# Optimization experiments

Measured on AMD Instinct MI355X. Metric: run time of the kernel, lower is better.

## Reference

```python
import jax, jax.numpy as jnp
import numpy as np
import math

B, T, C = 2, 2048, 1024
H = 16            # n_head
RATIO = 4         # ratio_kv
HKV = H // RATIO  # n_head_kv = 4
HD = C // H       # head_dim = 64
G = H // HKV      # query heads per kv head = 4


def _alibi_slopes(n_heads):
    # n_heads must be a power of 2 here (H=16)
    assert math.log2(n_heads).is_integer()
    start = 2.0 ** (-(2.0 ** (-(math.log2(n_heads) - 3))))
    return np.array([start * (start ** i) for i in range(n_heads)], dtype=np.float32)


def setup_inputs() -> dict:
    key = jax.random.key(0)
    ks = jax.random.split(key, 5)
    return {
        "x": jax.random.normal(ks[0], (B, T, C), dtype=jnp.float32),
        "Wq": jax.random.normal(ks[1], (C, C), dtype=jnp.float32) * 0.02,
        "Wk": jax.random.normal(ks[2], (C, HKV * HD), dtype=jnp.float32) * 0.02,
        "Wv": jax.random.normal(ks[3], (C, HKV * HD), dtype=jnp.float32) * 0.02,
        "Wo": jax.random.normal(ks[4], (C, C), dtype=jnp.float32) * 0.02,
    }


def reference(x, Wq, Wk, Wv, Wo):
    # GQA causal attention with ALiBi bias (flash-disabled fallback path).
    # q: [B,HKV,G,T,HD] (grouped query heads), k/v: [B,HKV,T,HD]
    q = (x @ Wq).reshape(B, T, H, HD).transpose(0, 2, 1, 3).reshape(B, HKV, G, T, HD)
    k = (x @ Wk).reshape(B, T, HKV, HD).transpose(0, 2, 1, 3)
    v = (x @ Wv).reshape(B, T, HKV, HD).transpose(0, 2, 1, 3)

    scale = 1.0 / math.sqrt(HD)
    att = jnp.einsum('bkgtd,bksd->bkgts', q, k) * scale  # [B,HKV,G,T,T]

    # ALiBi: original repeats alibi(n_head) by G and truncates to n_head,
    # so query head h uses slope get_slopes(H)[h // G] == slopes[:HKV] per kv group.
    slopes = jnp.asarray(_alibi_slopes(H))[:HKV]          # [HKV]
    pos = jnp.arange(T)
    rel = (pos[None, :] - pos[:, None]).astype(jnp.float32)  # [T,T], rel[i,j]=j-i
    bias = slopes[:, None, None] * rel                    # [HKV,T,T]
    causal = jnp.triu(jnp.full((T, T), -jnp.inf, dtype=jnp.float32), 1)

    att = att + bias[None, :, None] + causal
    att = jax.nn.softmax(att.astype(jnp.float32), axis=-1).astype(q.dtype)

    y = jnp.einsum('bkgts,bksd->bkgtd', att, v)           # [B,HKV,G,T,HD]
    y = y.reshape(B, H, T, HD).transpose(0, 2, 1, 3).reshape(B, T, C)
    return y @ Wo
```

## Files before the change

### kernel.cpp

```cpp
#include <hip/hip_runtime.h>
#include <hip/hip_bf16.h>
#include <math.h>

#define B_ 2
#define T_ 2048
#define C_ 1024
#define H_ 16
#define HKV_ 4
#define G_ 4
#define HD_ 64
#define KVC_ 256
#define NQKV_ 1536
#define NQT_ 32

typedef __attribute__((ext_vector_type(8))) short bf16x8;
typedef __attribute__((ext_vector_type(4))) float f32x4;

static __device__ inline short f2bf(float f) {
    __hip_bfloat16 h = __float2bfloat16(f);
    short s;
    __builtin_memcpy(&s, &h, 2);
    return s;
}
static __device__ inline short f2bf_trunc(float f) {
    unsigned int u;
    __builtin_memcpy(&u, &f, 4);
    return (short)(u >> 16);
}
static __device__ inline float bf2f(short s) {
    unsigned int u = ((unsigned int)(unsigned short)s) << 16;
    float f;
    __builtin_memcpy(&f, &u, 4);
    return f;
}

static __device__ inline void gload_lds16(const short* g, short* lds) {
    __builtin_amdgcn_global_load_lds(
        (const __attribute__((address_space(1))) unsigned int*)g,
        (__attribute__((address_space(3))) unsigned int*)lds, 16, 0, 0);
}

__global__ __launch_bounds__(256) void cast_bf16(
    const float* __restrict__ in, short* __restrict__ out, int n)
{
    const int i = (blockIdx.x * 256 + threadIdx.x) * 8;
    if (i >= n) return;
    const float4 a = *(const float4*)(in + i);
    const float4 b = *(const float4*)(in + i + 4);
    bf16x8 o;
    o[0] = f2bf(a.x); o[1] = f2bf(a.y); o[2] = f2bf(a.z); o[3] = f2bf(a.w);
    o[4] = f2bf(b.x); o[5] = f2bf(b.y); o[6] = f2bf(b.z); o[7] = f2bf(b.w);
    *(bf16x8*)(out + i) = o;
}

__global__ __launch_bounds__(256) void w_transpose(
    const float* __restrict__ Wq, const float* __restrict__ Wk,
    const float* __restrict__ Wv, const float* __restrict__ Wo,
    short* __restrict__ Wt, short* __restrict__ Wot)
{
    const int z = blockIdx.z;
    const float* in;
    short* out;
    int N;
    if (z == 0)      { in = Wq; out = Wt;                     N = C_; }
    else if (z == 1) { in = Wk; out = Wt + C_ * C_;           N = KVC_; }
    else if (z == 2) { in = Wv; out = Wt + (C_ + KVC_) * C_;  N = KVC_; }
    else             { in = Wo; out = Wot;                    N = C_; }
    const int n0 = blockIdx.x * 32;
    if (n0 >= N) return;
    __shared__ float t[32][33];
    const int tx = threadIdx.x, ty = threadIdx.y;
    const int k0 = blockIdx.y * 32;
    #pragma unroll
    for (int j = 0; j < 4; j++)
        t[ty + j * 8][tx] = in[(size_t)(k0 + ty + j * 8) * N + n0 + tx];
    __syncthreads();
    #pragma unroll
    for (int j = 0; j < 4; j++)
        out[(size_t)(n0 + ty + j * 8) * C_ + k0 + tx] = f2bf(t[tx][ty + j * 8]);
}

template <bool OUT_BF16>
__global__ __launch_bounds__(256) void gemm_bf16(
    const short* __restrict__ A, const short* __restrict__ Bt,
    void* __restrict__ Cout, int M, int N, int K)
{
    __shared__ short As[2][128 * 32];
    __shared__ short Bs[2][128 * 32];
    const int tid = threadIdx.x;
    const int wave = tid >> 6, lane = tid & 63;
    const int l15 = lane & 15, quad = lane >> 4;
    const int row0 = blockIdx.y * 128, col0 = blockIdx.x * 128;
    const int wr = (wave >> 1) * 64, wc = (wave & 1) * 64;
    const int sr = lane >> 2, kof = (lane & 3) * 8;

    f32x4 acc[4][4];
    #pragma unroll
    for (int i = 0; i < 4; i++)
        #pragma unroll
        for (int j = 0; j < 4; j++)
            acc[i][j] = (f32x4){0.f, 0.f, 0.f, 0.f};

#define GSTAGE(KT, BUF) do {                                                   \
        _Pragma("unroll")                                                      \
        for (int i_ = 0; i_ < 2; i_++) {                                       \
            const int rr = i_ * 64 + wave * 16;                                \
            gload_lds16(A + (size_t)(row0 + rr + sr) * K + (KT) + kof,         \
                        &As[BUF][rr * 32]);                                    \
            gload_lds16(Bt + (size_t)(col0 + rr + sr) * K + (KT) + kof,        \
                        &Bs[BUF][rr * 32]);                                    \
        }                                                                      \
    } while (0)

    GSTAGE(0, 0);
    asm volatile("s_waitcnt vmcnt(0)" ::: "memory");
    __builtin_amdgcn_s_barrier();

    int cur = 0;
    const int nkt = K >> 5;
    for (int t = 0; t < nkt; ++t) {
        if (t + 1 < nkt) GSTAGE((t + 1) * 32, cur ^ 1);

        bf16x8 af[4], bfr[4];
        #pragma unroll
        for (int mt = 0; mt < 4; mt++)
            af[mt] = *(const bf16x8*)&As[cur][(wr + mt * 16 + l15) * 32 + quad * 8];
        #pragma unroll
        for (int nt = 0; nt < 4; nt++)
            bfr[nt] = *(const bf16x8*)&Bs[cur][(wc + nt * 16 + l15) * 32 + quad * 8];
        #pragma unroll
        for (int mt = 0; mt < 4; mt++)
            #pragma unroll
            for (int nt = 0; nt < 4; nt++)
                acc[mt][nt] = __builtin_amdgcn_mfma_f32_16x16x32_bf16(
                    af[mt], bfr[nt], acc[mt][nt], 0, 0, 0);

        asm volatile("s_waitcnt vmcnt(0)" ::: "memory");
        __builtin_amdgcn_s_barrier();
        cur ^= 1;
    }
#undef GSTAGE

    #pragma unroll
    for (int mt = 0; mt < 4; mt++) {
        #pragma unroll
        for (int r = 0; r < 4; r++) {
            const size_t row = row0 + wr + mt * 16 + quad * 4 + r;
            #pragma unroll
            for (int nt = 0; nt < 4; nt++) {
                const size_t col = col0 + wc + nt * 16 + l15;
                if (OUT_BF16)
                    ((short*)Cout)[row * N + col] = f2bf(acc[mt][nt][r]);
                else
                    ((float*)Cout)[row * N + col] = acc[mt][nt][r];
            }
        }
    }
}

__global__ __launch_bounds__(256) void kv_tile(
    const short* __restrict__ QKV, short* __restrict__ Kt, short* __restrict__ Vt)
{
    __shared__ short Ls[64 * 72];
    const int jt = blockIdx.x;
    const int bk = blockIdx.y;
    const int b = bk >> 2, kh = bk & 3;
    const int tid = threadIdx.x;
    const int key = tid >> 2, d16 = (tid & 3) * 16;
    const size_t src = (size_t)(b * T_ + jt * 64 + key) * NQKV_ + C_ + kh * 64 + d16;
    const size_t tbase = (size_t)(bk * 32 + jt) * 4096;

    {
        const int i = (key >> 4) * 2 + (d16 >> 5);
        const int qd = (d16 & 31) >> 3;
        short* dst = Kt + tbase + i * 512 + (qd * 16 + (key & 15)) * 8;
        *(bf16x8*)dst         = *(const bf16x8*)(QKV + src);
        *(bf16x8*)(dst + 128) = *(const bf16x8*)(QKV + src + 8);
    }
    *(bf16x8*)&Ls[key * 72 + d16]     = *(const bf16x8*)(QKV + src + KVC_);
    *(bf16x8*)&Ls[key * 72 + d16 + 8] = *(const bf16x8*)(QKV + src + KVC_ + 8);
    __syncthreads();
    const int d = tid >> 2, k16 = (tid & 3) * 16;
    bf16x8 o0, o1;
    #pragma unroll
    for (int i = 0; i < 8; i++) o0[i] = Ls[(k16 + i) * 72 + d];
    #pragma unroll
    for (int i = 0; i < 8; i++) o1[i] = Ls[(k16 + 8 + i) * 72 + d];
    {
        const int i = (d >> 4) * 2 + (k16 >> 5);
        const int qk = (k16 & 31) >> 3;
        short* dst = Vt + tbase + i * 512 + (qk * 16 + (d & 15)) * 8;
        *(bf16x8*)dst         = o0;
        *(bf16x8*)(dst + 128) = o1;
    }
}

#define LSTR 72

__global__ __launch_bounds__(256, 4) void attn_mfma(
    const short* __restrict__ QKV, const short* __restrict__ Ktg,
    const short* __restrict__ Vtg, short* __restrict__ Y)
{
    const int qt = NQT_ - 1 - blockIdx.x;
    const int bh = blockIdx.y;
    const int b = bh >> 4, h = bh & 15, kh = h >> 2;
    const float slope2 = exp2f(-0.5f * (float)(kh + 1)) * 1.44269504f;
    const int tid = threadIdx.x;
    const int wave = tid >> 6, lane = tid & 63;
    const int l15 = lane & 15, quad = lane >> 4;

    __shared__ short Ps[4 * 16 * LSTR];
    short* Pw = &Ps[wave * 16 * LSTR];
    const int wswz = ((quad >> 1) & 1) << 4;
    const int rswz = ((l15 >> 3) & 1) << 4;

    const size_t bT = (size_t)b * T_;
    const size_t tb0 = (size_t)((b * HKV_ + kh) * 32) * 4096;
    const short* Kt = Ktg + tb0;
    const short* Vt = Vtg + tb0;
    const int qrow0 = qt * 64 + wave * 16;

    const float qscale = 0.125f * 1.44269504f;
    bf16x8 qf[2];
    #pragma unroll
    for (int k0 = 0; k0 < 2; k0++) {
        const short* qp = QKV + (bT + qrow0 + l15) * NQKV_ + h * 64;
        bf16x8 r = *(const bf16x8*)(qp + k0 * 32 + quad * 8);
        #pragma unroll
        for (int j = 0; j < 8; j++)
            qf[k0][j] = f2bf(bf2f(r[j]) * qscale);
    }

    const short one_s = (short)0x3F80;
    const bf16x8 ones = {one_s, one_s, one_s, one_s, one_s, one_s, one_s, one_s};

    f32x4 Oacc[4], lacc;
    #pragma unroll
    for (int nt = 0; nt < 4; nt++)
        Oacc[nt] = (f32x4){0.f, 0.f, 0.f, 0.f};
    lacc = (f32x4){0.f, 0.f, 0.f, 0.f};

    bf16x8 kf[8], vf[8];
    #pragma unroll
    for (int i = 0; i < 8; i++)
        kf[i] = *(const bf16x8*)(Kt + i * 512 + lane * 8);
    #pragma unroll
    for (int i = 0; i < 8; i++)
        vf[i] = *(const bf16x8*)(Vt + i * 512 + lane * 8);

    for (int jtk = 0; jtk <= qt; jtk++) {
        const int pjt = (jtk < qt) ? jtk + 1 : qt;

        f32x4 s[4];
        #pragma unroll
        for (int nt = 0; nt < 4; nt++) {
            f32x4 a = {0.f, 0.f, 0.f, 0.f};
            a = __builtin_amdgcn_mfma_f32_16x16x32_bf16(qf[0], kf[nt*2+0], a, 0, 0, 0);
            a = __builtin_amdgcn_mfma_f32_16x16x32_bf16(qf[1], kf[nt*2+1], a, 0, 0, 0);
            s[nt] = a;
        }

        #pragma unroll
        for (int i = 0; i < 8; i++)
            kf[i] = *(const bf16x8*)(Kt + (size_t)pjt * 4096 + i * 512 + lane * 8);

        {
            const float base = slope2 * (float)(jtk * 64 + l15 - quad * 4 - qrow0);
            if (jtk == qt) {
                #pragma unroll
                for (int nt = 0; nt < 4; nt++) {
                    const int colsw = ((nt * 16 + l15) ^ wswz);
                    #pragma unroll
                    for (int r = 0; r < 4; r++) {
                        const float relv = (float)(jtk * 64 + l15 - quad * 4 - qrow0)
                                         + (float)(nt * 16 - r);
                        float p = __builtin_amdgcn_exp2f(
                            fmaf(slope2, (float)(nt * 16 - r), base) + s[nt][r]);
                        if (relv > 0.f) p = 0.f;
                        Pw[(quad * 4 + r) * LSTR + colsw] = f2bf_trunc(p);
                    }
                }
            } else {
                #pragma unroll
                for (int nt = 0; nt < 4; nt++) {
                    const int colsw = ((nt * 16 + l15) ^ wswz);
                    #pragma unroll
                    for (int r = 0; r < 4; r++) {
                        float p = __builtin_amdgcn_exp2f(
                            fmaf(slope2, (float)(nt * 16 - r), base) + s[nt][r]);
                        Pw[(quad * 4 + r) * LSTR + colsw] = f2bf_trunc(p);
                    }
                }
            }
        }
        __asm__ volatile("s_waitcnt lgkmcnt(0)" ::: "memory");

        {
            bf16x8 pf0 = *(const bf16x8*)&Pw[l15 * LSTR + ((quad * 8) ^ rswz)];
            bf16x8 pf1 = *(const bf16x8*)&Pw[l15 * LSTR + ((32 + quad * 8) ^ rswz)];
            lacc = __builtin_amdgcn_mfma_f32_16x16x32_bf16(pf0, ones, lacc, 0, 0, 0);
            lacc = __builtin_amdgcn_mfma_f32_16x16x32_bf16(pf1, ones, lacc, 0, 0, 0);
            #pragma unroll
            for (int nt = 0; nt < 4; nt++) {
                Oacc[nt] = __builtin_amdgcn_mfma_f32_16x16x32_bf16(
                    pf0, vf[nt*2+0], Oacc[nt], 0, 0, 0);
                Oacc[nt] = __builtin_amdgcn_mfma_f32_16x16x32_bf16(
                    pf1, vf[nt*2+1], Oacc[nt], 0, 0, 0);
            }
        }

        #pragma unroll
        for (int i = 0; i < 8; i++)
            vf[i] = *(const bf16x8*)(Vt + (size_t)pjt * 4096 + i * 512 + lane * 8);
    }

    #pragma unroll
    for (int r = 0; r < 4; r++) {
        const float inv = 1.f / lacc[r];
        const int row = qrow0 + quad * 4 + r;
        short* yp = Y + (bT + row) * C_ + h * 64 + l15;
        #pragma unroll
        for (int nt = 0; nt < 4; nt++)
            yp[nt * 16] = f2bf(Oacc[nt][r] * inv);
    }
}

extern "C" void kernel_launch(void* const* d_in, const int* in_sizes, int n_in,
                              void* d_out, int out_size, void* d_ws, size_t ws_size,
                              hipStream_t stream) {
    const float* x  = (const float*)d_in[0];
    const float* Wq = (const float*)d_in[1];
    const float* Wk = (const float*)d_in[2];
    const float* Wv = (const float*)d_in[3];
    const float* Wo = (const float*)d_in[4];
    float* out = (float*)d_out;

    const int M = B_ * T_;
    short* xb  = (short*)d_ws;
    short* Wt  = xb  + (size_t)M * C_;
    short* Wot = Wt  + (size_t)NQKV_ * C_;
    short* QKV = Wot + (size_t)C_ * C_;
    short* Yb  = QKV + (size_t)M * NQKV_;
    short* Ktg = Yb  + (size_t)M * C_;
    short* Vtg = Ktg + (size_t)8 * 32 * 4096;

    cast_bf16<<<dim3(M * C_ / (256 * 8)), dim3(256), 0, stream>>>(x, xb, M * C_);
    w_transpose<<<dim3(32, 32, 4), dim3(32, 8), 0, stream>>>(Wq, Wk, Wv, Wo, Wt, Wot);

    gemm_bf16<true><<<dim3(NQKV_ / 128, M / 128), dim3(256), 0, stream>>>(
        xb, Wt, QKV, M, NQKV_, C_);
    kv_tile<<<dim3(32, 8), dim3(256), 0, stream>>>(QKV, Ktg, Vtg);
    attn_mfma<<<dim3(NQT_, B_ * H_), dim3(256), 0, stream>>>(QKV, Ktg, Vtg, Yb);
    gemm_bf16<false><<<dim3(C_ / 128, M / 128), dim3(256), 0, stream>>>(
        Yb, Wot, out, M, C_, C_);
}
```

Before: 198.7 us.

## Process two query heads per attention block to share K/V fragment loads

Each attention block now handles two query heads of the same KV group, so every K and V fragment loaded into registers feeds twice as many MFMAs. The grid's y dimension is halved, and the per-wave P buffer in shared memory doubles to hold both heads' probabilities. The intent is to cut K/V global traffic per unit of compute and amortize the load latency. The cost is higher register pressure from the doubled accumulators, with the launch-bounds occupancy hint dropped, and half as many blocks in the grid.

```diff
diff --git a/kernel.cpp b/kernel.cpp
--- a/kernel.cpp
+++ b/kernel.cpp
@@ -197,20 +197,21 @@
 
 #define LSTR 72
 
-__global__ __launch_bounds__(256, 4) void attn_mfma(
+__global__ __launch_bounds__(256) void attn_mfma(
     const short* __restrict__ QKV, const short* __restrict__ Ktg,
     const short* __restrict__ Vtg, short* __restrict__ Y)
 {
     const int qt = NQT_ - 1 - blockIdx.x;
-    const int bh = blockIdx.y;
-    const int b = bh >> 4, h = bh & 15, kh = h >> 2;
+    const int byp = blockIdx.y;
+    const int b = byp >> 3, kh = (byp >> 1) & 3, hp = byp & 1;
+    const int h0 = kh * 4 + hp * 2;
     const float slope2 = exp2f(-0.5f * (float)(kh + 1)) * 1.44269504f;
     const int tid = threadIdx.x;
     const int wave = tid >> 6, lane = tid & 63;
     const int l15 = lane & 15, quad = lane >> 4;
 
-    __shared__ short Ps[4 * 16 * LSTR];
-    short* Pw = &Ps[wave * 16 * LSTR];
+    __shared__ short Ps[4 * 32 * LSTR];
+    short* Pw = &Ps[wave * 32 * LSTR];
     const int wswz = ((quad >> 1) & 1) << 4;
     const int rswz = ((l15 >> 3) & 1) << 4;
 
@@ -221,24 +222,30 @@
     const int qrow0 = qt * 64 + wave * 16;
 
     const float qscale = 0.125f * 1.44269504f;
-    bf16x8 qf[2];
+    bf16x8 qf0[2], qf1[2];
     #pragma unroll
     for (int k0 = 0; k0 < 2; k0++) {
-        const short* qp = QKV + (bT + qrow0 + l15) * NQKV_ + h * 64;
-        bf16x8 r = *(const bf16x8*)(qp + k0 * 32 + quad * 8);
-        #pragma unroll
-        for (int j = 0; j < 8; j++)
-            qf[k0][j] = f2bf(bf2f(r[j]) * qscale);
+        const short* qp = QKV + (bT + qrow0 + l15) * NQKV_ + h0 * 64;
+        bf16x8 r0 = *(const bf16x8*)(qp + k0 * 32 + quad * 8);
+        bf16x8 r1 = *(const bf16x8*)(qp + 64 + k0 * 32 + quad * 8);
+        #pragma unroll
+        for (int j = 0; j < 8; j++) {
+            qf0[k0][j] = f2bf(bf2f(r0[j]) * qscale);
+            qf1[k0][j] = f2bf(bf2f(r1[j]) * qscale);
+        }
     }
 
     const short one_s = (short)0x3F80;
     const bf16x8 ones = {one_s, one_s, one_s, one_s, one_s, one_s, one_s, one_s};
 
-    f32x4 Oacc[4], lacc;
-    #pragma unroll
-    for (int nt = 0; nt < 4; nt++)
-        Oacc[nt] = (f32x4){0.f, 0.f, 0.f, 0.f};
-    lacc = (f32x4){0.f, 0.f, 0.f, 0.f};
+    f32x4 Oacc0[4], Oacc1[4], lacc0, lacc1;
+    #pragma unroll
+    for (int nt = 0; nt < 4; nt++) {
+        Oacc0[nt] = (f32x4){0.f, 0.f, 0.f, 0.f};
+        Oacc1[nt] = (f32x4){0.f, 0.f, 0.f, 0.f};
+    }
+    lacc0 = (f32x4){0.f, 0.f, 0.f, 0.f};
+    lacc1 = (f32x4){0.f, 0.f, 0.f, 0.f};
 
     bf16x8 kf[8], vf[8];
     #pragma unroll
@@ -251,45 +258,54 @@
     for (int jtk = 0; jtk <= qt; jtk++) {
         const int pjt = (jtk < qt) ? jtk + 1 : qt;
 
-        f32x4 s[4];
+        f32x4 s0[4], s1[4];
         #pragma unroll
         for (int nt = 0; nt < 4; nt++) {
             f32x4 a = {0.f, 0.f, 0.f, 0.f};
-            a = __builtin_amdgcn_mfma_f32_16x16x32_bf16(qf[0], kf[nt*2+0], a, 0, 0, 0);
-            a = __builtin_amdgcn_mfma_f32_16x16x32_bf16(qf[1], kf[nt*2+1], a, 0, 0, 0);
-            s[nt] = a;
+            a = __builtin_amdgcn_mfma_f32_16x16x32_bf16(qf0[0], kf[nt*2+0], a, 0, 0, 0);
+            a = __builtin_amdgcn_mfma_f32_16x16x32_bf16(qf0[1], kf[nt*2+1], a, 0, 0, 0);
+            s0[nt] = a;
+        }
+        #pragma unroll
+        for (int nt = 0; nt < 4; nt++) {
+            f32x4 a = {0.f, 0.f, 0.f, 0.f};
+            a = __builtin_amdgcn_mfma_f32_16x16x32_bf16(qf1[0], kf[nt*2+0], a, 0, 0, 0);
+            a = __builtin_amdgcn_mfma_f32_16x16x32_bf16(qf1[1], kf[nt*2+1], a, 0, 0, 0);
+            s1[nt] = a;
         }
 
         #pragma unroll
         for (int i = 0; i < 8; i++)
             kf[i] = *(const bf16x8*)(Kt + (size_t)pjt * 4096 + i * 512 + lane * 8);
 
-        {
-            const float base = slope2 * (float)(jtk * 64 + l15 - quad * 4 - qrow0);
-            if (jtk == qt) {
+        const float base = slope2 * (float)(jtk * 64 + l15 - quad * 4 - qrow0);
+        if (jtk == qt) {
+            #pragma unroll
+            for (int nt = 0; nt < 4; nt++) {
+                const int colsw = ((nt * 16 + l15) ^ wswz);
                 #pragma unroll
-                for (int nt = 0; nt < 4; nt++) {
-                    const int colsw = ((nt * 16 + l15) ^ wswz);
-                    #pragma unroll
-                    for (int r = 0; r < 4; r++) {
-                        const float relv = (float)(jtk * 64 + l15 - quad * 4 - qrow0)
-                                         + (float)(nt * 16 - r);
-                        float p = __builtin_amdgcn_exp2f(
-                            fmaf(slope2, (float)(nt * 16 - r), base) + s[nt][r]);
-                        if (relv > 0.f) p = 0.f;
-                        Pw[(quad * 4 + r) * LSTR + colsw] = f2bf_trunc(p);
-                    }
+                for (int r = 0; r < 4; r++) {
+                    const float relv = (float)(jtk * 64 + l15 - quad * 4 - qrow0)
+                                     + (float)(nt * 16 - r);
+                    const float bb = fmaf(slope2, (float)(nt * 16 - r), base);
+                    float p0 = __builtin_amdgcn_exp2f(bb + s0[nt][r]);
+                    float p1 = __builtin_amdgcn_exp2f(bb + s1[nt][r]);
+                    if (relv > 0.f) { p0 = 0.f; p1 = 0.f; }
+                    Pw[(quad * 4 + r) * LSTR + colsw]        = f2bf_trunc(p0);
+                    Pw[(16 + quad * 4 + r) * LSTR + colsw]   = f2bf_trunc(p1);
                 }
-            } else {
+            }
+        } else {
+            #pragma unroll
+            for (int nt = 0; nt < 4; nt++) {
+                const int colsw = ((nt * 16 + l15) ^ wswz);
                 #pragma unroll
-                for (int nt = 0; nt < 4; nt++) {
-                    const int colsw = ((nt * 16 + l15) ^ wswz);
-                    #pragma unroll
-                    for (int r = 0; r < 4; r++) {
-                        float p = __builtin_amdgcn_exp2f(
-                            fmaf(slope2, (float)(nt * 16 - r), base) + s[nt][r]);
-                        Pw[(quad * 4 + r) * LSTR + colsw] = f2bf_trunc(p);
-                    }
+                for (int r = 0; r < 4; r++) {
+                    const float bb = fmaf(slope2, (float)(nt * 16 - r), base);
+                    Pw[(quad * 4 + r) * LSTR + colsw] =
+                        f2bf_trunc(__builtin_amdgcn_exp2f(bb + s0[nt][r]));
+                    Pw[(16 + quad * 4 + r) * LSTR + colsw] =
+                        f2bf_trunc(__builtin_amdgcn_exp2f(bb + s1[nt][r]));
                 }
             }
         }
@@ -298,14 +314,27 @@
         {
             bf16x8 pf0 = *(const bf16x8*)&Pw[l15 * LSTR + ((quad * 8) ^ rswz)];
             bf16x8 pf1 = *(const bf16x8*)&Pw[l15 * LSTR + ((32 + quad * 8) ^ rswz)];
-            lacc = __builtin_amdgcn_mfma_f32_16x16x32_bf16(pf0, ones, lacc, 0, 0, 0);
-            lacc = __builtin_amdgcn_mfma_f32_16x16x32_bf16(pf1, ones, lacc, 0, 0, 0);
-            #pragma unroll
-            for (int nt = 0; nt < 4; nt++) {
-                Oacc[nt] = __builtin_amdgcn_mfma_f32_16x16x32_bf16(
-                    pf0, vf[nt*2+0], Oacc[nt], 0, 0, 0);
-                Oacc[nt] = __builtin_amdgcn_mfma_f32_16x16x32_bf16(
-                    pf1, vf[nt*2+1], Oacc[nt], 0, 0, 0);
+            lacc0 = __builtin_amdgcn_mfma_f32_16x16x32_bf16(pf0, ones, lacc0, 0, 0, 0);
+            lacc0 = __builtin_amdgcn_mfma_f32_16x16x32_bf16(pf1, ones, lacc0, 0, 0, 0);
+            #pragma unroll
+            for (int nt = 0; nt < 4; nt++) {
+                Oacc0[nt] = __builtin_amdgcn_mfma_f32_16x16x32_bf16(
+                    pf0, vf[nt*2+0], Oacc0[nt], 0, 0, 0);
+                Oacc0[nt] = __builtin_amdgcn_mfma_f32_16x16x32_bf16(
+                    pf1, vf[nt*2+1], Oacc0[nt], 0, 0, 0);
+            }
+        }
+        {
+            bf16x8 pf0 = *(const bf16x8*)&Pw[(16 + l15) * LSTR + ((quad * 8) ^ rswz)];
+            bf16x8 pf1 = *(const bf16x8*)&Pw[(16 + l15) * LSTR + ((32 + quad * 8) ^ rswz)];
+            lacc1 = __builtin_amdgcn_mfma_f32_16x16x32_bf16(pf0, ones, lacc1, 0, 0, 0);
+            lacc1 = __builtin_amdgcn_mfma_f32_16x16x32_bf16(pf1, ones, lacc1, 0, 0, 0);
+            #pragma unroll
+            for (int nt = 0; nt < 4; nt++) {
+                Oacc1[nt] = __builtin_amdgcn_mfma_f32_16x16x32_bf16(
+                    pf0, vf[nt*2+0], Oacc1[nt], 0, 0, 0);
+                Oacc1[nt] = __builtin_amdgcn_mfma_f32_16x16x32_bf16(
+                    pf1, vf[nt*2+1], Oacc1[nt], 0, 0, 0);
             }
         }
 
@@ -316,12 +345,15 @@
 
     #pragma unroll
     for (int r = 0; r < 4; r++) {
-        const float inv = 1.f / lacc[r];
+        const float inv0 = 1.f / lacc0[r];
+        const float inv1 = 1.f / lacc1[r];
         const int row = qrow0 + quad * 4 + r;
-        short* yp = Y + (bT + row) * C_ + h * 64 + l15;
-        #pragma unroll
-        for (int nt = 0; nt < 4; nt++)
-            yp[nt * 16] = f2bf(Oacc[nt][r] * inv);
+        short* yp = Y + (bT + row) * C_ + h0 * 64 + l15;
+        #pragma unroll
+        for (int nt = 0; nt < 4; nt++) {
+            yp[nt * 16]      = f2bf(Oacc0[nt][r] * inv0);
+            yp[64 + nt * 16] = f2bf(Oacc1[nt][r] * inv1);
+        }
     }
 }
 
@@ -350,7 +382,7 @@
     gemm_bf16<true><<<dim3(NQKV_ / 128, M / 128), dim3(256), 0, stream>>>(
         xb, Wt, QKV, M, NQKV_, C_);
     kv_tile<<<dim3(32, 8), dim3(256), 0, stream>>>(QKV, Ktg, Vtg);
-    attn_mfma<<<dim3(NQT_, B_ * H_), dim3(256), 0, stream>>>(QKV, Ktg, Vtg, Yb);
+    attn_mfma<<<dim3(NQT_, B_ * H_ / 2), dim3(256), 0, stream>>>(QKV, Ktg, Vtg, Yb);
     gemm_bf16<false><<<dim3(C_ / 128, M / 128), dim3(256), 0, stream>>>(
         Yb, Wot, out, M, C_, C_);
 }
```

New measurement: 175.1 us. 1.14x faster.

## Pair causal query tiles per block and software-pipeline QK with softmax/PV

Applied to the files above, without the earlier changes.

Each attention block now handles two query tiles, a high one (qtH) and a low one (qtL = 31 - qtH), so every block does the same amount of causal work and each loaded K/V tile serves both query tiles. The loop is unrolled by two with ping-pong score buffers, so the QK^T MFMAs for the next key tile are issued before the P·V MFMAs of the current one. s_setprio hints are placed around the MFMA groups. This raises register use (launch bounds drop to 2 blocks per CU) and halves the grid, which risks lower occupancy and fewer blocks in flight.

```diff
diff --git a/kernel.cpp b/kernel.cpp
--- a/kernel.cpp
+++ b/kernel.cpp
@@ -197,20 +197,148 @@
 
 #define LSTR 72
 
-__global__ __launch_bounds__(256, 4) void attn_mfma(
+#define ATTN_ITER(J, SCURH, SCURL, SNXTH, SNXTL)                               \
+  {                                                                            \
+    const int j_ = (J);                                                        \
+    const bool doL_ = (j_ <= qtL);                                             \
+                                                     \
+    {                                                                          \
+        const float base = slope2 * (float)(j_ * 64 + l15 - quad * 4 - qrow0H);\
+        if (j_ == qtH) {                                                       \
+            _Pragma("unroll")                                                  \
+            for (int nt = 0; nt < 4; nt++) {                                   \
+                const int colsw = ((nt * 16 + l15) ^ wswz);                    \
+                _Pragma("unroll")                                              \
+                for (int r = 0; r < 4; r++) {                                  \
+                    const float relv = (float)(j_ * 64 + l15 - quad * 4 - qrow0H)\
+                                     + (float)(nt * 16 - r);                   \
+                    float p = __builtin_amdgcn_exp2f(                          \
+                        fmaf(slope2, (float)(nt * 16 - r), base) + SCURH[nt][r]);\
+                    if (relv > 0.f) p = 0.f;                                   \
+                    Pw[(quad * 4 + r) * LSTR + colsw] = f2bf_trunc(p);         \
+                }                                                              \
+            }                                                                  \
+        } else {                                                               \
+            _Pragma("unroll")                                                  \
+            for (int nt = 0; nt < 4; nt++) {                                   \
+                const int colsw = ((nt * 16 + l15) ^ wswz);                    \
+                _Pragma("unroll")                                              \
+                for (int r = 0; r < 4; r++) {                                  \
+                    float p = __builtin_amdgcn_exp2f(                          \
+                        fmaf(slope2, (float)(nt * 16 - r), base) + SCURH[nt][r]);\
+                    Pw[(quad * 4 + r) * LSTR + colsw] = f2bf_trunc(p);         \
+                }                                                              \
+            }                                                                  \
+        }                                                                      \
+    }                                                                          \
+    if (doL_) {                                                                \
+        const float base = slope2 * (float)(j_ * 64 + l15 - quad * 4 - qrow0L);\
+        if (j_ == qtL) {                                                       \
+            _Pragma("unroll")                                                  \
+            for (int nt = 0; nt < 4; nt++) {                                   \
+                const int colsw = ((nt * 16 + l15) ^ wswz);                    \
+                _Pragma("unroll")                                              \
+                for (int r = 0; r < 4; r++) {                                  \
+                    const float relv = (float)(j_ * 64 + l15 - quad * 4 - qrow0L)\
+                                     + (float)(nt * 16 - r);                   \
+                    float p = __builtin_amdgcn_exp2f(                          \
+                        fmaf(slope2, (float)(nt * 16 - r), base) + SCURL[nt][r]);\
+                    if (relv > 0.f) p = 0.f;                                   \
+                    Pw[(16 + quad * 4 + r) * LSTR + colsw] = f2bf_trunc(p);    \
+                }                                                              \
+            }                                                                  \
+        } else {                                                               \
+            _Pragma("unroll")                                                  \
+            for (int nt = 0; nt < 4; nt++) {                                   \
+                const int colsw = ((nt * 16 + l15) ^ wswz);                    \
+                _Pragma("unroll")                                              \
+                for (int r = 0; r < 4; r++) {                                  \
+                    float p = __builtin_amdgcn_exp2f(                          \
+                        fmaf(slope2, (float)(nt * 16 - r), base) + SCURL[nt][r]);\
+                    Pw[(16 + quad * 4 + r) * LSTR + colsw] = f2bf_trunc(p);    \
+                }                                                              \
+            }                                                                  \
+        }                                                                      \
+    }                                                                          \
+                    \
+    if (j_ < qtH) {                                                            \
+        const bool doLn_ = (j_ + 1 <= qtL);                                    \
+        __builtin_amdgcn_s_setprio(1);                                         \
+        _Pragma("unroll")                                                      \
+        for (int nt = 0; nt < 4; nt++) {                                       \
+            f32x4 a = {0.f, 0.f, 0.f, 0.f};                                    \
+            a = __builtin_amdgcn_mfma_f32_16x16x32_bf16(qfH[0], kf[nt*2+0], a, 0, 0, 0);\
+            a = __builtin_amdgcn_mfma_f32_16x16x32_bf16(qfH[1], kf[nt*2+1], a, 0, 0, 0);\
+            SNXTH[nt] = a;                                                     \
+        }                                                                      \
+        if (doLn_) {                                                           \
+            _Pragma("unroll")                                                  \
+            for (int nt = 0; nt < 4; nt++) {                                   \
+                f32x4 a = {0.f, 0.f, 0.f, 0.f};                                \
+                a = __builtin_amdgcn_mfma_f32_16x16x32_bf16(qfL[0], kf[nt*2+0], a, 0, 0, 0);\
+                a = __builtin_amdgcn_mfma_f32_16x16x32_bf16(qfL[1], kf[nt*2+1], a, 0, 0, 0);\
+                SNXTL[nt] = a;                                                 \
+            }                                                                  \
+        }                                                                      \
+        __builtin_amdgcn_s_setprio(0);                                         \
+        const int pk_ = (j_ + 2 <= qtH) ? j_ + 2 : qtH;                        \
+        _Pragma("unroll")                                                      \
+        for (int i = 0; i < 8; i++)                                            \
+            kf[i] = *(const bf16x8*)(Kt + (size_t)pk_ * 4096 + i * 512 + lane * 8);\
+    }                                                                          \
+    __asm__ volatile("s_waitcnt lgkmcnt(0)" ::: "memory");                     \
+                                            \
+    {                                                                          \
+        bf16x8 pf0 = *(const bf16x8*)&Pw[l15 * LSTR + ((quad * 8) ^ rswz)];    \
+        bf16x8 pf1 = *(const bf16x8*)&Pw[l15 * LSTR + ((32 + quad * 8) ^ rswz)];\
+        __builtin_amdgcn_s_setprio(1);                                         \
+        laccH = __builtin_amdgcn_mfma_f32_16x16x32_bf16(pf0, ones, laccH, 0, 0, 0);\
+        laccH = __builtin_amdgcn_mfma_f32_16x16x32_bf16(pf1, ones, laccH, 0, 0, 0);\
+        _Pragma("unroll")                                                      \
+        for (int nt = 0; nt < 4; nt++) {                                       \
+            OaccH[nt] = __builtin_amdgcn_mfma_f32_16x16x32_bf16(               \
+                pf0, vf[nt*2+0], OaccH[nt], 0, 0, 0);                          \
+            OaccH[nt] = __builtin_amdgcn_mfma_f32_16x16x32_bf16(               \
+                pf1, vf[nt*2+1], OaccH[nt], 0, 0, 0);                          \
+        }                                                                      \
+        __builtin_amdgcn_s_setprio(0);                                         \
+    }                                                                          \
+    if (doL_) {                                                                \
+        bf16x8 pf0 = *(const bf16x8*)&Pw[(16 + l15) * LSTR + ((quad * 8) ^ rswz)];\
+        bf16x8 pf1 = *(const bf16x8*)&Pw[(16 + l15) * LSTR + ((32 + quad * 8) ^ rswz)];\
+        __builtin_amdgcn_s_setprio(1);                                         \
+        laccL = __builtin_amdgcn_mfma_f32_16x16x32_bf16(pf0, ones, laccL, 0, 0, 0);\
+        laccL = __builtin_amdgcn_mfma_f32_16x16x32_bf16(pf1, ones, laccL, 0, 0, 0);\
+        _Pragma("unroll")                                                      \
+        for (int nt = 0; nt < 4; nt++) {                                       \
+            OaccL[nt] = __builtin_amdgcn_mfma_f32_16x16x32_bf16(               \
+                pf0, vf[nt*2+0], OaccL[nt], 0, 0, 0);                          \
+            OaccL[nt] = __builtin_amdgcn_mfma_f32_16x16x32_bf16(               \
+                pf1, vf[nt*2+1], OaccL[nt], 0, 0, 0);                          \
+        }                                                                      \
+        __builtin_amdgcn_s_setprio(0);                                         \
+    }                                                                          \
+    const int pv_ = (j_ + 1 <= qtH) ? j_ + 1 : qtH;                            \
+    _Pragma("unroll")                                                          \
+    for (int i = 0; i < 8; i++)                                                \
+        vf[i] = *(const bf16x8*)(Vt + (size_t)pv_ * 4096 + i * 512 + lane * 8);\
+  }
+
+__global__ __launch_bounds__(256, 2) void attn_mfma(
     const short* __restrict__ QKV, const short* __restrict__ Ktg,
     const short* __restrict__ Vtg, short* __restrict__ Y)
 {
-    const int qt = NQT_ - 1 - blockIdx.x;
+    const int qx = blockIdx.x;
     const int bh = blockIdx.y;
+    const int qtL = qx, qtH = NQT_ - 1 - qx;
     const int b = bh >> 4, h = bh & 15, kh = h >> 2;
     const float slope2 = exp2f(-0.5f * (float)(kh + 1)) * 1.44269504f;
     const int tid = threadIdx.x;
     const int wave = tid >> 6, lane = tid & 63;
     const int l15 = lane & 15, quad = lane >> 4;
 
-    __shared__ short Ps[4 * 16 * LSTR];
-    short* Pw = &Ps[wave * 16 * LSTR];
+    __shared__ short Ps[4 * 32 * LSTR];
+    short* Pw = &Ps[wave * 32 * LSTR];
     const int wswz = ((quad >> 1) & 1) << 4;
     const int rswz = ((l15 >> 3) & 1) << 4;
 
@@ -218,27 +346,35 @@
     const size_t tb0 = (size_t)((b * HKV_ + kh) * 32) * 4096;
     const short* Kt = Ktg + tb0;
     const short* Vt = Vtg + tb0;
-    const int qrow0 = qt * 64 + wave * 16;
+    const int qrow0H = qtH * 64 + wave * 16;
+    const int qrow0L = qtL * 64 + wave * 16;
 
     const float qscale = 0.125f * 1.44269504f;
-    bf16x8 qf[2];
+    bf16x8 qfH[2], qfL[2];
     #pragma unroll
     for (int k0 = 0; k0 < 2; k0++) {
-        const short* qp = QKV + (bT + qrow0 + l15) * NQKV_ + h * 64;
-        bf16x8 r = *(const bf16x8*)(qp + k0 * 32 + quad * 8);
-        #pragma unroll
-        for (int j = 0; j < 8; j++)
-            qf[k0][j] = f2bf(bf2f(r[j]) * qscale);
+        const short* qpH = QKV + (bT + qrow0H + l15) * NQKV_ + h * 64;
+        const short* qpL = QKV + (bT + qrow0L + l15) * NQKV_ + h * 64;
+        bf16x8 rH = *(const bf16x8*)(qpH + k0 * 32 + quad * 8);
+        bf16x8 rL = *(const bf16x8*)(qpL + k0 * 32 + quad * 8);
+        #pragma unroll
+        for (int j = 0; j < 8; j++) {
+            qfH[k0][j] = f2bf(bf2f(rH[j]) * qscale);
+            qfL[k0][j] = f2bf(bf2f(rL[j]) * qscale);
+        }
     }
 
     const short one_s = (short)0x3F80;
     const bf16x8 ones = {one_s, one_s, one_s, one_s, one_s, one_s, one_s, one_s};
 
-    f32x4 Oacc[4], lacc;
-    #pragma unroll
-    for (int nt = 0; nt < 4; nt++)
-        Oacc[nt] = (f32x4){0.f, 0.f, 0.f, 0.f};
-    lacc = (f32x4){0.f, 0.f, 0.f, 0.f};
+    f32x4 OaccH[4], OaccL[4], laccH, laccL;
+    #pragma unroll
+    for (int nt = 0; nt < 4; nt++) {
+        OaccH[nt] = (f32x4){0.f, 0.f, 0.f, 0.f};
+        OaccL[nt] = (f32x4){0.f, 0.f, 0.f, 0.f};
+    }
+    laccH = (f32x4){0.f, 0.f, 0.f, 0.f};
+    laccL = (f32x4){0.f, 0.f, 0.f, 0.f};
 
     bf16x8 kf[8], vf[8];
     #pragma unroll
@@ -248,80 +384,46 @@
     for (int i = 0; i < 8; i++)
         vf[i] = *(const bf16x8*)(Vt + i * 512 + lane * 8);
 
-    for (int jtk = 0; jtk <= qt; jtk++) {
-        const int pjt = (jtk < qt) ? jtk + 1 : qt;
-
-        f32x4 s[4];
+    f32x4 sAH[4], sAL[4], sBH[4], sBL[4];
+    #pragma unroll
+    for (int nt = 0; nt < 4; nt++) {
+        f32x4 a = {0.f, 0.f, 0.f, 0.f};
+        a = __builtin_amdgcn_mfma_f32_16x16x32_bf16(qfH[0], kf[nt*2+0], a, 0, 0, 0);
+        a = __builtin_amdgcn_mfma_f32_16x16x32_bf16(qfH[1], kf[nt*2+1], a, 0, 0, 0);
+        sAH[nt] = a;
+    }
+    #pragma unroll
+    for (int nt = 0; nt < 4; nt++) {
+        f32x4 a = {0.f, 0.f, 0.f, 0.f};
+        a = __builtin_amdgcn_mfma_f32_16x16x32_bf16(qfL[0], kf[nt*2+0], a, 0, 0, 0);
+        a = __builtin_amdgcn_mfma_f32_16x16x32_bf16(qfL[1], kf[nt*2+1], a, 0, 0, 0);
+        sAL[nt] = a;
+    }
+    {
+        #pragma unroll
+        for (int i = 0; i < 8; i++)
+            kf[i] = *(const bf16x8*)(Kt + (size_t)4096 + i * 512 + lane * 8);
+    }
+
+    for (int j = 0; j <= qtH; j += 2) {
+        ATTN_ITER(j, sAH, sAL, sBH, sBL);
+        if (j + 1 <= qtH)
+            ATTN_ITER(j + 1, sBH, sBL, sAH, sAL);
+    }
+
+    #pragma unroll
+    for (int r = 0; r < 4; r++) {
+        const float invH = 1.f / laccH[r];
+        const float invL = 1.f / laccL[r];
+        const int rowH = qrow0H + quad * 4 + r;
+        const int rowL = qrow0L + quad * 4 + r;
+        short* ypH = Y + (bT + rowH) * C_ + h * 64 + l15;
+        short* ypL = Y + (bT + rowL) * C_ + h * 64 + l15;
         #pragma unroll
         for (int nt = 0; nt < 4; nt++) {
-            f32x4 a = {0.f, 0.f, 0.f, 0.f};
-            a = __builtin_amdgcn_mfma_f32_16x16x32_bf16(qf[0], kf[nt*2+0], a, 0, 0, 0);
-            a = __builtin_amdgcn_mfma_f32_16x16x32_bf16(qf[1], kf[nt*2+1], a, 0, 0, 0);
-            s[nt] = a;
+            ypH[nt * 16] = f2bf(OaccH[nt][r] * invH);
+            ypL[nt * 16] = f2bf(OaccL[nt][r] * invL);
         }
-
-        #pragma unroll
-        for (int i = 0; i < 8; i++)
-            kf[i] = *(const bf16x8*)(Kt + (size_t)pjt * 4096 + i * 512 + lane * 8);
-
-        {
-            const float base = slope2 * (float)(jtk * 64 + l15 - quad * 4 - qrow0);
-            if (jtk == qt) {
-                #pragma unroll
-                for (int nt = 0; nt < 4; nt++) {
-                    const int colsw = ((nt * 16 + l15) ^ wswz);
-                    #pragma unroll
-                    for (int r = 0; r < 4; r++) {
-                        const float relv = (float)(jtk * 64 + l15 - quad * 4 - qrow0)
-                                         + (float)(nt * 16 - r);
-                        float p = __builtin_amdgcn_exp2f(
-                            fmaf(slope2, (float)(nt * 16 - r), base) + s[nt][r]);
-                        if (relv > 0.f) p = 0.f;
-                        Pw[(quad * 4 + r) * LSTR + colsw] = f2bf_trunc(p);
-                    }
-                }
-            } else {
-                #pragma unroll
-                for (int nt = 0; nt < 4; nt++) {
-                    const int colsw = ((nt * 16 + l15) ^ wswz);
-                    #pragma unroll
-                    for (int r = 0; r < 4; r++) {
-                        float p = __builtin_amdgcn_exp2f(
-                            fmaf(slope2, (float)(nt * 16 - r), base) + s[nt][r]);
-                        Pw[(quad * 4 + r) * LSTR + colsw] = f2bf_trunc(p);
-                    }
-                }
-            }
-        }
-        __asm__ volatile("s_waitcnt lgkmcnt(0)" ::: "memory");
-
-        {
-            bf16x8 pf0 = *(const bf16x8*)&Pw[l15 * LSTR + ((quad * 8) ^ rswz)];
-            bf16x8 pf1 = *(const bf16x8*)&Pw[l15 * LSTR + ((32 + quad * 8) ^ rswz)];
-            lacc = __builtin_amdgcn_mfma_f32_16x16x32_bf16(pf0, ones, lacc, 0, 0, 0);
-            lacc = __builtin_amdgcn_mfma_f32_16x16x32_bf16(pf1, ones, lacc, 0, 0, 0);
-            #pragma unroll
-            for (int nt = 0; nt < 4; nt++) {
-                Oacc[nt] = __builtin_amdgcn_mfma_f32_16x16x32_bf16(
-                    pf0, vf[nt*2+0], Oacc[nt], 0, 0, 0);
-                Oacc[nt] = __builtin_amdgcn_mfma_f32_16x16x32_bf16(
-                    pf1, vf[nt*2+1], Oacc[nt], 0, 0, 0);
-            }
-        }
-
-        #pragma unroll
-        for (int i = 0; i < 8; i++)
-            vf[i] = *(const bf16x8*)(Vt + (size_t)pjt * 4096 + i * 512 + lane * 8);
-    }
-
-    #pragma unroll
-    for (int r = 0; r < 4; r++) {
-        const float inv = 1.f / lacc[r];
-        const int row = qrow0 + quad * 4 + r;
-        short* yp = Y + (bT + row) * C_ + h * 64 + l15;
-        #pragma unroll
-        for (int nt = 0; nt < 4; nt++)
-            yp[nt * 16] = f2bf(Oacc[nt][r] * inv);
     }
 }
 
@@ -350,7 +452,7 @@
     gemm_bf16<true><<<dim3(NQKV_ / 128, M / 128), dim3(256), 0, stream>>>(
         xb, Wt, QKV, M, NQKV_, C_);
     kv_tile<<<dim3(32, 8), dim3(256), 0, stream>>>(QKV, Ktg, Vtg);
-    attn_mfma<<<dim3(NQT_, B_ * H_), dim3(256), 0, stream>>>(QKV, Ktg, Vtg, Yb);
+    attn_mfma<<<dim3(NQT_ / 2, B_ * H_), dim3(256), 0, stream>>>(QKV, Ktg, Vtg, Yb);
     gemm_bf16<false><<<dim3(C_ / 128, M / 128), dim3(256), 0, stream>>>(
         Yb, Wot, out, M, C_, C_);
 }
```

Result: faster. 170.0 us (-14.4%).
